# Optimization experiments

Measured on AMD Instinct MI355X. Metric: run time of the kernel, lower is better.

## Reference

```python
import jax, jax.numpy as jnp
import numpy as np

UNITS, N, S = 256, 64, 4
BATCH, T = 64, 1024


def setup_inputs() -> dict:
    key = jax.random.key(0)
    k0, k1, k2, k3 = jax.random.split(key, 4)
    return {
        "inputs": jax.random.uniform(k0, (BATCH, T, S), dtype=jnp.float32),
        "transition_kernel": jax.random.normal(k1, (UNITS, N, N), dtype=jnp.float32),
        "emission_kernel": jax.random.normal(k2, (UNITS, N, S), dtype=jnp.float32),
        "init_kernel": jax.random.normal(k3, (UNITS, N), dtype=jnp.float32),
    }


def reference(inputs, transition_kernel, emission_kernel, init_kernel):
    # Softmaxed HMM parameters (computed once; the TF cell recomputes per step).
    A = jax.nn.softmax(transition_kernel, axis=-1)  # [U, N, N] transitions
    B = jax.nn.softmax(emission_kernel, axis=-1)    # [U, N, S] emissions
    I = jax.nn.softmax(init_kernel, axis=-1)        # [U, N]    initial dist

    batch = inputs.shape[0]
    U, Nn = init_kernel.shape

    alpha0 = jnp.zeros((batch, U, Nn), dtype=inputs.dtype)
    ll0 = jnp.zeros((batch, U), dtype=inputs.dtype)
    is_init0 = jnp.ones((batch,), dtype=inputs.dtype)  # HMM starts in init at t=0

    def step(carry, x_t):
        alpha, ll, is_init = carry
        # R[b,u,j] = is_init[b]*I[u,j] + sum_i A[u,i,j]*alpha[b,u,i]  (A^T matvec)
        R = is_init[:, None, None] * I[None] + jnp.einsum("uij,bui->buj", A, alpha)
        # E[b,u,i] = sum_c B[u,i,c] * x_t[b,c]
        E = jnp.einsum("unc,bc->bun", B, x_t)
        fwd = E * R                              # [B, U, N]
        Ssum = jnp.sum(fwd, axis=-1)             # [B, U]
        ll = ll + jnp.log(Ssum)
        alpha = fwd / Ssum[..., None]            # normalized forward variable
        return (alpha, ll, jnp.zeros_like(is_init)), ll

    xs = jnp.swapaxes(inputs, 0, 1)  # [T, B, S]
    (_, _, _), lls = jax.lax.scan(step, (alpha0, ll0, is_init0), xs)
    # whole-sequence output: cumulative log-likelihood per step, [B, T, U]
    return jnp.swapaxes(lls, 0, 1)
```

## Files before the change

kernel.cpp:

```cpp
#include <hip/hip_runtime.h>


#define U_ 256
#define N_ 64
#define S_ 4
#define B_ 64
#define T_ 1024
#define ROWP 72
#define LN2F 0.69314718055994530942f

typedef __attribute__((ext_vector_type(8))) __bf16 bf16x8;
typedef __attribute__((ext_vector_type(4))) float floatx4;

__device__ __forceinline__ int sig(int jt, int m) {
    return 32 * (jt >> 1) + 4 * (jt & 1) + 8 * (m >> 2) + (m & 3);
}

__launch_bounds__(256, 1)
__global__ void hmm_fwd_kernel(const float* __restrict__ xg,
                               const float* __restrict__ trans,
                               const float* __restrict__ emis,
                               const float* __restrict__ initk,
                               float* __restrict__ out)
{
    __shared__ __bf16 AT[N_ * ROWP];
    __shared__ float BemS[N_][S_];
    __shared__ float IS[N_];

    const int bid = blockIdx.x;
    const int u = ((bid & 7) << 5) | (bid >> 3);
    const int tid = threadIdx.x;
    const int lane = tid & 63;
    const int w = tid >> 6;
    const int q = lane >> 4;
    const int l = lane & 15;

    if (tid < 64) {
        const float* rowp = trans + (u * N_ + tid) * N_;
        float v[N_];
        #pragma unroll
        for (int k = 0; k < 16; ++k) {
            floatx4 t4 = *(const floatx4*)(rowp + 4 * k);
            v[4*k] = t4.x; v[4*k+1] = t4.y; v[4*k+2] = t4.z; v[4*k+3] = t4.w;
        }
        float m = v[0];
        #pragma unroll
        for (int j = 1; j < N_; ++j) m = fmaxf(m, v[j]);
        float s = 0.f;
        #pragma unroll
        for (int j = 0; j < N_; ++j) { v[j] = __expf(v[j] - m); s += v[j]; }
        float inv = 1.0f / s;
        #pragma unroll
        for (int j = 0; j < N_; ++j) AT[j * ROWP + tid] = (__bf16)(v[j] * inv);
    } else if (tid < 128) {
        int n = tid - 64;
        floatx4 e4 = *(const floatx4*)(emis + (u * N_ + n) * S_);
        float m = fmaxf(fmaxf(e4.x, e4.y), fmaxf(e4.z, e4.w));
        float a = __expf(e4.x - m), b2 = __expf(e4.y - m);
        float c = __expf(e4.z - m), d = __expf(e4.w - m);
        float inv = 1.0f / (a + b2 + c + d);
        BemS[n][0] = a*inv; BemS[n][1] = b2*inv; BemS[n][2] = c*inv; BemS[n][3] = d*inv;
    } else if (tid < 192) {
        int j = tid - 128;
        float v = initk[u * N_ + j];
        float m = v;
        #pragma unroll
        for (int s = 1; s < 64; s <<= 1) m = fmaxf(m, __shfl_xor(m, s, 64));
        float e = __expf(v - m);
        float ssum = e;
        #pragma unroll
        for (int s = 1; s < 64; s <<= 1) ssum += __shfl_xor(ssum, s, 64);
        IS[j] = e / ssum;
    }
    __syncthreads();

    bf16x8 afrag[4][2];
    #pragma unroll
    for (int jt = 0; jt < 4; ++jt)
        #pragma unroll
        for (int kt = 0; kt < 2; ++kt)
            afrag[jt][kt] = *(const bf16x8*)&AT[sig(jt, l) * ROWP + 32*kt + 8*q];

    floatx4 cBem[4][4];
    #pragma unroll
    for (int jt = 0; jt < 4; ++jt)
        #pragma unroll
        for (int r = 0; r < 4; ++r)
            cBem[jt][r] = *(const floatx4*)&BemS[sig(jt, 4*q + r)][0];

    floatx4 Rv[4];
    #pragma unroll
    for (int jt = 0; jt < 4; ++jt)
        #pragma unroll
        for (int r = 0; r < 4; ++r) Rv[jt][r] = IS[sig(jt, 4*q + r)];

    __asm__ volatile("" ::: "memory");

    const int b = 16*w + l;
    const float* xin = xg + b * (T_ * S_);
    float* llout = out + (size_t)b * T_ * U_ + u;

    const floatx4 z = {0.f, 0.f, 0.f, 0.f};

    auto emitE = [&](floatx4* Edst, const floatx4& xr) {
        #pragma unroll
        for (int jt = 0; jt < 4; ++jt) {
            #pragma unroll
            for (int r = 0; r < 4; ++r) {
                const floatx4 cb = cBem[jt][r];
                Edst[jt][r] = fmaf(cb.x, xr.x,
                              fmaf(cb.y, xr.y,
                              fmaf(cb.z, xr.z, cb.w * xr.w)));
            }
        }
    };

    floatx4 Ev[4];
    emitE(Ev, *(const floatx4*)xin);

    floatx4 xvA[4], xvB[4];
    #pragma unroll
    for (int i = 0; i < 4; ++i)
        xvA[i] = *(const floatx4*)(xin + (1 + i) * S_);

    float hist[8];
    float ssf = 1.0f;
    float pp0 = 0.f, pa16 = 0.f, pa32 = 0.f, pa48 = 0.f;
    float Cacc = 0.f;
    float offacc = 0.f, sumk = 0.f;

    auto consume = [&](int kprev, bool o) {
        float ss = (pp0 + pa16) + (pa32 + pa48);
        hist[kprev] = o ? ss : hist[kprev];
        if (kprev == 5) ssf = ss;
    };

    auto step = [&](const floatx4& xr, int slot, bool own, bool ownP) {
        floatx4 gv[4];
        #pragma unroll
        for (int jt = 0; jt < 4; ++jt) gv[jt] = Ev[jt] * Rv[jt];

        bf16x8 bf0, bf1;
        #pragma unroll
        for (int p = 0; p < 4; ++p) {
            bf0[p]     = (__bf16)gv[0][p];
            bf0[4 + p] = (__bf16)gv[1][p];
            bf1[p]     = (__bf16)gv[2][p];
            bf1[4 + p] = (__bf16)gv[3][p];
        }

        #pragma unroll
        for (int jt = 0; jt < 4; ++jt) {
            floatx4 acc = __builtin_amdgcn_mfma_f32_16x16x32_bf16(afrag[jt][0], bf0, z, 0, 0, 0);
            Rv[jt] = __builtin_amdgcn_mfma_f32_16x16x32_bf16(afrag[jt][1], bf1, acc, 0, 0, 0);
        }

        if (slot == 0) consume(7, ownP); else consume(slot - 1, own);

        emitE(Ev, xr);

        floatx4 s4 = (gv[0] + gv[1]) + (gv[2] + gv[3]);
        pp0  = (s4.x + s4.y) + (s4.z + s4.w);
        pa16 = __shfl_xor(pp0, 16, 64);
        pa32 = __shfl_xor(pp0, 32, 64);
        pa48 = __shfl_xor(pp0, 48, 64);
    };

    #pragma unroll 1
    for (int tb = 0; tb < T_; tb += 8) {
        const int oct = (tb >> 3) & 3;
        const bool own  = (q == oct);
        const bool ownP = (q == ((oct + 3) & 3));

        #pragma unroll
        for (int i = 0; i < 4; ++i) {
            int ti = tb + 5 + i; ti = (ti < T_) ? ti : T_ - 1;
            xvB[i] = *(const floatx4*)(xin + ti * S_);
        }

        step(xvA[0], 0, own, ownP); step(xvA[1], 1, own, ownP);
        step(xvA[2], 2, own, ownP); step(xvA[3], 3, own, ownP);

        #pragma unroll
        for (int i = 0; i < 4; ++i) {
            int ti = tb + 9 + i; ti = (ti < T_) ? ti : T_ - 1;
            xvA[i] = *(const floatx4*)(xin + ti * S_);
        }

        step(xvB[0], 4, own, ownP); step(xvB[1], 5, own, ownP);
        step(xvB[2], 6, own, ownP); step(xvB[3], 7, own, ownP);

        if (oct == 3) consume(7, own);

        {
            unsigned eb = (__float_as_uint(ssf) >> 23) & 255u;
            float f = __uint_as_float((254u - eb) << 23);
            #pragma unroll
            for (int jt = 0; jt < 4; ++jt) Rv[jt] *= f;
            float kf = (float)((int)eb - 127);
            offacc += (q > oct) ? kf : 0.f;
            sumk   += kf;
        }

        if (oct == 3) {
            float base = Cacc + LN2F * offacc;
            float* fp = llout + (size_t)(tb - 24 + 8 * q) * U_;
            #pragma unroll
            for (int k = 0; k < 8; ++k)
                fp[(size_t)k * U_] = __logf(hist[k]) + base;
            Cacc += LN2F * sumk;
            offacc = 0.f; sumk = 0.f;
        }
    }
}

extern "C" void kernel_launch(void* const* d_in, const int* in_sizes, int n_in,
                              void* d_out, int out_size, void* d_ws, size_t ws_size,
                              hipStream_t stream) {
    const float* xg    = (const float*)d_in[0];
    const float* trans = (const float*)d_in[1];
    const float* emis  = (const float*)d_in[2];
    const float* initk = (const float*)d_in[3];
    float* out = (float*)d_out;
    hipLaunchKernelGGL(hmm_fwd_kernel, dim3(U_), dim3(256), 0, stream,
                       xg, trans, emis, initk, out);
}
```

Before: 364.7 us.

## Split MFMA accumulation chains, fold rescale into emission, and interleave via sched barriers

Each output tile's two dependent MFMAs become two independent MFMAs whose results are summed at the next step, which shortens the serial dependency chain. The emission values are double-buffered, and the per-octet power-of-two rescale factor is folded into the next emission input instead of a separate multiply on R. sched_group_barrier hints interleave the MFMAs with the emission FMAs to hide MFMA latency. In exchange each step adds a vector add and more registers, and the hand-set schedule counts may not match the instructions the compiler actually emits.

```diff
diff --git a/kernel.cpp b/kernel.cpp
--- a/kernel.cpp
+++ b/kernel.cpp
@@ -11,6 +11,8 @@
 
 typedef __attribute__((ext_vector_type(8))) __bf16 bf16x8;
 typedef __attribute__((ext_vector_type(4))) float floatx4;
+
+#define SGB __builtin_amdgcn_sched_group_barrier
 
 __device__ __forceinline__ int sig(int jt, int m) {
     return 32 * (jt >> 1) + 4 * (jt & 1) + 8 * (m >> 2) + (m & 3);
@@ -88,11 +90,14 @@
         for (int r = 0; r < 4; ++r)
             cBem[jt][r] = *(const floatx4*)&BemS[sig(jt, 4*q + r)][0];
 
-    floatx4 Rv[4];
+    floatx4 P0[4], P1[4];
     #pragma unroll
     for (int jt = 0; jt < 4; ++jt)
         #pragma unroll
-        for (int r = 0; r < 4; ++r) Rv[jt][r] = IS[sig(jt, 4*q + r)];
+        for (int r = 0; r < 4; ++r) {
+            P0[jt][r] = IS[sig(jt, 4*q + r)];
+            P1[jt][r] = 0.f;
+        }
 
     __asm__ volatile("" ::: "memory");
 
@@ -102,21 +107,19 @@
 
     const floatx4 z = {0.f, 0.f, 0.f, 0.f};
 
-    auto emitE = [&](floatx4* Edst, const floatx4& xr) {
-        #pragma unroll
-        for (int jt = 0; jt < 4; ++jt) {
-            #pragma unroll
-            for (int r = 0; r < 4; ++r) {
-                const floatx4 cb = cBem[jt][r];
-                Edst[jt][r] = fmaf(cb.x, xr.x,
-                              fmaf(cb.y, xr.y,
-                              fmaf(cb.z, xr.z, cb.w * xr.w)));
-            }
-        }
+    auto dot4 = [](const floatx4& cb, const floatx4& x4) {
+        return fmaf(cb.x, x4.x, fmaf(cb.y, x4.y, fmaf(cb.z, x4.z, cb.w * x4.w)));
     };
 
-    floatx4 Ev[4];
-    emitE(Ev, *(const floatx4*)xin);
+    floatx4 EvA[4], EvB[4];
+    {
+        floatx4 x0 = *(const floatx4*)xin;
+        #pragma unroll
+        for (int jt = 0; jt < 4; ++jt)
+            #pragma unroll
+            for (int r = 0; r < 4; ++r)
+                EvA[jt][r] = dot4(cBem[jt][r], x0);
+    }
 
     floatx4 xvA[4], xvB[4];
     #pragma unroll
@@ -125,6 +128,7 @@
 
     float hist[8];
     float ssf = 1.0f;
+    float fcur = 1.0f;
     float pp0 = 0.f, pa16 = 0.f, pa32 = 0.f, pa48 = 0.f;
     float Cacc = 0.f;
     float offacc = 0.f, sumk = 0.f;
@@ -132,14 +136,21 @@
     auto consume = [&](int kprev, bool o) {
         float ss = (pp0 + pa16) + (pa32 + pa48);
         hist[kprev] = o ? ss : hist[kprev];
-        if (kprev == 5) ssf = ss;
+        if (kprev == 5) {
+            ssf = ss;
+            unsigned eb = (__float_as_uint(ss) >> 23) & 255u;
+            fcur = __uint_as_float((254u - eb) << 23);
+        }
     };
 
-    auto step = [&](const floatx4& xr, int slot, bool own, bool ownP) {
+    auto step = [&](const floatx4& xnx, int slot, bool own, bool ownP,
+                    const floatx4* Ein, floatx4* Eout, float fs) {
         floatx4 gv[4];
         #pragma unroll
-        for (int jt = 0; jt < 4; ++jt) gv[jt] = Ev[jt] * Rv[jt];
-
+        for (int jt = 0; jt < 4; ++jt) {
+            floatx4 Rv = P0[jt] + P1[jt];
+            gv[jt] = Ein[jt] * Rv;
+        }
         bf16x8 bf0, bf1;
         #pragma unroll
         for (int p = 0; p < 4; ++p) {
@@ -149,21 +160,44 @@
             bf1[4 + p] = (__bf16)gv[3][p];
         }
 
-        #pragma unroll
-        for (int jt = 0; jt < 4; ++jt) {
-            floatx4 acc = __builtin_amdgcn_mfma_f32_16x16x32_bf16(afrag[jt][0], bf0, z, 0, 0, 0);
-            Rv[jt] = __builtin_amdgcn_mfma_f32_16x16x32_bf16(afrag[jt][1], bf1, acc, 0, 0, 0);
-        }
+        P0[0] = __builtin_amdgcn_mfma_f32_16x16x32_bf16(afrag[0][0], bf0, z, 0, 0, 0);
+        P1[0] = __builtin_amdgcn_mfma_f32_16x16x32_bf16(afrag[0][1], bf1, z, 0, 0, 0);
 
         if (slot == 0) consume(7, ownP); else consume(slot - 1, own);
 
-        emitE(Ev, xr);
+        P0[1] = __builtin_amdgcn_mfma_f32_16x16x32_bf16(afrag[1][0], bf0, z, 0, 0, 0);
+        P1[1] = __builtin_amdgcn_mfma_f32_16x16x32_bf16(afrag[1][1], bf1, z, 0, 0, 0);
+
+        floatx4 xs = xnx * fs;
+        #pragma unroll
+        for (int jt = 0; jt < 2; ++jt)
+            #pragma unroll
+            for (int r = 0; r < 4; ++r)
+                Eout[jt][r] = dot4(cBem[jt][r], xs);
+
+        P0[2] = __builtin_amdgcn_mfma_f32_16x16x32_bf16(afrag[2][0], bf0, z, 0, 0, 0);
+        P1[2] = __builtin_amdgcn_mfma_f32_16x16x32_bf16(afrag[2][1], bf1, z, 0, 0, 0);
+
+        #pragma unroll
+        for (int jt = 2; jt < 4; ++jt)
+            #pragma unroll
+            for (int r = 0; r < 4; ++r)
+                Eout[jt][r] = dot4(cBem[jt][r], xs);
+
+        P0[3] = __builtin_amdgcn_mfma_f32_16x16x32_bf16(afrag[3][0], bf0, z, 0, 0, 0);
+        P1[3] = __builtin_amdgcn_mfma_f32_16x16x32_bf16(afrag[3][1], bf1, z, 0, 0, 0);
 
         floatx4 s4 = (gv[0] + gv[1]) + (gv[2] + gv[3]);
         pp0  = (s4.x + s4.y) + (s4.z + s4.w);
         pa16 = __shfl_xor(pp0, 16, 64);
         pa32 = __shfl_xor(pp0, 32, 64);
         pa48 = __shfl_xor(pp0, 48, 64);
+
+        SGB(0x2, 40, 0);
+        SGB(0x8, 2, 0); SGB(0x2, 8, 0);
+        SGB(0x8, 2, 0); SGB(0x2, 32, 0);
+        SGB(0x8, 2, 0); SGB(0x2, 32, 0);
+        SGB(0x8, 2, 0); SGB(0x2, 12, 0);
     };
 
     #pragma unroll 1
@@ -178,8 +212,10 @@
             xvB[i] = *(const floatx4*)(xin + ti * S_);
         }
 
-        step(xvA[0], 0, own, ownP); step(xvA[1], 1, own, ownP);
-        step(xvA[2], 2, own, ownP); step(xvA[3], 3, own, ownP);
+        step(xvA[0], 0, own, ownP, EvA, EvB, 1.0f);
+        step(xvA[1], 1, own, ownP, EvB, EvA, 1.0f);
+        step(xvA[2], 2, own, ownP, EvA, EvB, 1.0f);
+        step(xvA[3], 3, own, ownP, EvB, EvA, 1.0f);
 
         #pragma unroll
         for (int i = 0; i < 4; ++i) {
@@ -187,16 +223,15 @@
             xvA[i] = *(const floatx4*)(xin + ti * S_);
         }
 
-        step(xvB[0], 4, own, ownP); step(xvB[1], 5, own, ownP);
-        step(xvB[2], 6, own, ownP); step(xvB[3], 7, own, ownP);
+        step(xvB[0], 4, own, ownP, EvA, EvB, 1.0f);
+        step(xvB[1], 5, own, ownP, EvB, EvA, 1.0f);
+        step(xvB[2], 6, own, ownP, EvA, EvB, 1.0f);
+        step(xvB[3], 7, own, ownP, EvB, EvA, fcur);
 
         if (oct == 3) consume(7, own);
 
         {
             unsigned eb = (__float_as_uint(ssf) >> 23) & 255u;
-            float f = __uint_as_float((254u - eb) << 23);
-            #pragma unroll
-            for (int jt = 0; jt < 4; ++jt) Rv[jt] *= f;
             float kf = (float)((int)eb - 127);
             offacc += (q > oct) ? kf : 0.f;
             sumk   += kf;
```

After: 486.9 us. +33.5%, slower.
